# Kernel optimization log

Measured on AMD Instinct MI355X. Metric: run time of the kernel, lower is better.

Reference implementation:

```python
import jax, jax.numpy as jnp
import numpy as np

TEMPERATURE = 0.1
TIME_THRESHOLD = 365
NEG = -1e9  # stands in for -inf; exp(NEG - max) == 0 exactly in fp32
EPS = 1e-12  # F.normalize eps


def setup_inputs() -> dict:
    key = jax.random.key(0)
    k1, k2, k3 = jax.random.split(key, 3)
    B, D = 8192, 128
    embeddings = jax.random.normal(k1, (B, D), dtype=jnp.float32)
    survival_times = jax.random.randint(k2, (B,), 0, 3650, dtype=jnp.int32)
    censor = jax.random.randint(k3, (B,), 0, 2, dtype=jnp.int32)
    return {"embeddings": embeddings, "survival_times": survival_times, "censor": censor}


def reference(embeddings, survival_times, censor):
    B = embeddings.shape[0]
    # L2 normalize rows (torch F.normalize semantics)
    norm = jnp.maximum(jnp.linalg.norm(embeddings, axis=1, keepdims=True), EPS)
    z = embeddings / norm
    # pairwise cosine similarity / temperature: [B, B]
    sim = jnp.einsum('ik,jk->ij', z, z) / TEMPERATURE
    diag = jnp.eye(B, dtype=bool)
    sim = jnp.where(diag, NEG, sim)  # mask self-similarity
    # positive mask: |t_i - t_j| < threshold, i != j, row i uncensored
    tdiff = jnp.abs(survival_times[:, None] - survival_times[None, :])
    pos = (tdiff < TIME_THRESHOLD) & (~diag) & (censor[:, None] == 1)
    # per-row masked logsumexp reductions
    denominator = jax.nn.logsumexp(sim, axis=1)                      # [B]
    numerator = jax.nn.logsumexp(jnp.where(pos, sim, NEG), axis=1)   # [B]
    has_pos = jnp.any(pos, axis=1)
    per_row = jnp.where(has_pos, denominator - numerator, 0.0)
    cnt = jnp.sum(has_pos.astype(jnp.float32))
    return jnp.where(cnt > 0, jnp.sum(per_row) / jnp.maximum(cnt, 1.0), 0.0)
```

## Files before the change

kernel.cpp:

```cpp
#include <hip/hip_runtime.h>
#include <cstdint>

#define BDIM 8192
#define DDIM 128
#define JS 32

#define ZH_OFF 0
#define ZL_OFF (2 * 1024 * 1024)
#define RL_OFF (4 * 1024 * 1024)
#define CNT_OFF (RL_OFF + BDIM * 4)
#define FC_OFF (CNT_OFF + 64)
#define P_OFF (RL_OFF + 65536)
#define PART_OFF (P_OFF + BDIM * JS * 8)

typedef __attribute__((ext_vector_type(8))) short bf16x8;
typedef __attribute__((ext_vector_type(4))) float f32x4;

__device__ __forceinline__ short f2bf(float f) {
  unsigned u = __float_as_uint(f);
  unsigned r = (u + 0x7fffu + ((u >> 16) & 1u)) >> 16;
  return (short)r;
}
__device__ __forceinline__ float bf2f(short h) {
  return __uint_as_float(((unsigned)(unsigned short)h) << 16);
}
__device__ __forceinline__ void gload_lds16(const void* g, void* l) {
  __builtin_amdgcn_global_load_lds(
      (const __attribute__((address_space(1))) unsigned int*)g,
      (__attribute__((address_space(3))) unsigned int*)l, 16, 0, 0);
}


__global__ __launch_bounds__(256) void ck_prep(
    const float* __restrict__ emb, const int* __restrict__ censor,
    short* __restrict__ ZhT, short* __restrict__ ZlT,
    int* __restrict__ rowlist, int* __restrict__ cnt, int* __restrict__ fc)
{
  __shared__ float zl[16][132];
  __shared__ float pr[16][16];
  __shared__ float inv[16];
  __shared__ int wtot[4], woff[4];

  const int t = threadIdx.x;
  if (blockIdx.x == 512) {
    const int lane = t & 63, wv = t >> 6;
    const int4* c4 = (const int4*)(censor + t * 32);
    unsigned fm = 0;
#pragma unroll
    for (int q = 0; q < 8; ++q) {
      const int4 v = c4[q];
      fm |= (unsigned)(v.x == 1) << (q * 4 + 0);
      fm |= (unsigned)(v.y == 1) << (q * 4 + 1);
      fm |= (unsigned)(v.z == 1) << (q * 4 + 2);
      fm |= (unsigned)(v.w == 1) << (q * 4 + 3);
    }
    const int loc = __popc(fm);
    int sc = loc;
#pragma unroll
    for (int m = 1; m < 64; m <<= 1) {
      const int u = __shfl_up(sc, m, 64);
      if (lane >= m) sc += u;
    }
    if (lane == 63) wtot[wv] = sc;
    __syncthreads();
    if (t == 0) {
      int run = 0;
#pragma unroll
      for (int i = 0; i < 4; ++i) { woff[i] = run; run += wtot[i]; }
      fc[0] = 0;
    }
    __syncthreads();
    int off = woff[wv] + sc - loc;
    for (int u = 0; u < 32; ++u)
      if ((fm >> u) & 1) rowlist[off++] = t * 32 + u;
    if (t == 255) cnt[0] = off;
    return;
  }

  const int R = blockIdx.x;
  const int r16 = t >> 4, seg = t & 15;
  const float4* src = (const float4*)(emb + (size_t)(R * 16 + r16) * DDIM + seg * 8);
  const float4 v0 = src[0], v1 = src[1];
  float* zr = &zl[r16][seg * 8];
  zr[0] = v0.x; zr[1] = v0.y; zr[2] = v0.z; zr[3] = v0.w;
  zr[4] = v1.x; zr[5] = v1.y; zr[6] = v1.z; zr[7] = v1.w;
  pr[r16][seg] = v0.x * v0.x + v0.y * v0.y + v0.z * v0.z + v0.w * v0.w +
                 v1.x * v1.x + v1.y * v1.y + v1.z * v1.z + v1.w * v1.w;
  __syncthreads();
  if (t < 16) {
    float ss = 0.f;
#pragma unroll
    for (int s = 0; s < 16; ++s) ss += pr[t][s];
    inv[t] = 1.0f / fmaxf(sqrtf(ss), 1e-12f);
  }
  __syncthreads();
  const int kc = t >> 6, hf = (t >> 4) & 3, rw = t & 15;
  const float iv = inv[rw];
  const float* zs = &zl[rw][(kc * 4 + hf) * 8];
  short hs[8], ls[8];
#pragma unroll
  for (int j = 0; j < 8; ++j) {
    const float z = zs[j] * iv;
    const short h = f2bf(z);
    hs[j] = h;
    ls[j] = f2bf(z - bf2f(h));
  }
  const int dst = R * 2048 + t * 8;
  *(bf16x8*)(ZhT + dst) = *(const bf16x8*)hs;
  *(bf16x8*)(ZlT + dst) = *(const bf16x8*)ls;
}

__global__ __launch_bounds__(256, 2) void ck_main(
    const short* __restrict__ ZhT, const short* __restrict__ ZlT,
    const int* __restrict__ rowlist, const int* __restrict__ cntp,
    const int* __restrict__ times, float2* __restrict__ P2)
{
  __shared__ __align__(16) char lds[65536];
  const int cnt = *cntp;
  const int t = threadIdx.x;
  const int b = blockIdx.x;
  const int it = b >> 5;
  const int js = b & 31;
  if (it * 128 >= cnt) return;
  const int lane = t & 63;
  const int w = t >> 6;
  const int half = lane >> 4;
  const int ll = lane & 15;
  const int jR0 = js * 16;

  int rbase[2];
#pragma unroll
  for (int a = 0; a < 2; ++a) {
    int c = it * 128 + w * 32 + a * 16 + ll;
    if (c >= cnt) c = cnt - 1;
    const int r = rowlist[c];
    rbase[a] = (r >> 4) * 2048 + (r & 15) * 8;
  }
  bf16x8 ah[2][4];
#pragma unroll
  for (int a = 0; a < 2; ++a)
#pragma unroll
    for (int kc = 0; kc < 4; ++kc)
      ah[a][kc] = *(const bf16x8*)(ZhT + rbase[a] + kc * 512 + half * 128);

  int meta[2][4];
#pragma unroll
  for (int a = 0; a < 2; ++a)
#pragma unroll
    for (int r = 0; r < 4; ++r) {
      const int idx = it * 128 + w * 32 + a * 16 + half * 4 + r;
      const bool vi = idx < cnt;
      const int gi = rowlist[vi ? idx : 0];
      const int taP = vi ? (times[gi] + 364) : 50000;
      meta[a][r] = (taP << 16) | (vi ? gi : 0xFFFF);
    }

  float sd[2][4] = {{0.f}}, sn[2][4] = {{0.f}};

  {
    const int c0 = w * 8;
#pragma unroll
    for (int u = 0; u < 8; ++u) {
      const int c = c0 + u, cp = c & 15;
      const short* src = (c < 16) ? ZhT : ZlT;
      const short* gp = src + (size_t)(jR0 + (cp >> 2)) * 2048 + (cp & 3) * 512 + lane * 8;
      gload_lds16(gp, lds + ((c < 16) ? 0 : 16384) + cp * 1024);
    }
  }

  for (int st = 0; st < 4; ++st) {
    __syncthreads();
    if (st < 3) {
      const int pB = ((st + 1) & 1) * 32768;
      const int c0 = w * 8;
#pragma unroll
      for (int u = 0; u < 8; ++u) {
        const int c = c0 + u, cp = c & 15;
        const short* src = (c < 16) ? ZhT : ZlT;
        const short* gp = src + (size_t)(jR0 + (st + 1) * 4 + (cp >> 2)) * 2048 + (cp & 3) * 512 + lane * 8;
        gload_lds16(gp, lds + pB + ((c < 16) ? 0 : 16384) + cp * 1024);
      }
    }

    const char* L = lds + (st & 1) * 32768;
    f32x4 acc[2][4];
#pragma unroll
    for (int a = 0; a < 2; ++a)
#pragma unroll
      for (int bb = 0; bb < 4; ++bb) acc[a][bb] = (f32x4){0.f, 0.f, 0.f, 0.f};

#pragma unroll
    for (int kc = 0; kc < 4; ++kc) {
      bf16x8 alv[2];
#pragma unroll
      for (int a = 0; a < 2; ++a)
        alv[a] = *(const bf16x8*)(ZlT + rbase[a] + kc * 512 + half * 128);
#pragma unroll
      for (int bb = 0; bb < 4; ++bb) {
        const bf16x8 bhv = *(const bf16x8*)(L + bb * 4096 + kc * 1024 + lane * 16);
        const bf16x8 blv = *(const bf16x8*)(L + 16384 + bb * 4096 + kc * 1024 + lane * 16);
        acc[0][bb] = __builtin_amdgcn_mfma_f32_16x16x32_bf16(ah[0][kc], bhv, acc[0][bb], 0, 0, 0);
        acc[1][bb] = __builtin_amdgcn_mfma_f32_16x16x32_bf16(ah[1][kc], bhv, acc[1][bb], 0, 0, 0);
        acc[0][bb] = __builtin_amdgcn_mfma_f32_16x16x32_bf16(ah[0][kc], blv, acc[0][bb], 0, 0, 0);
        acc[1][bb] = __builtin_amdgcn_mfma_f32_16x16x32_bf16(ah[1][kc], blv, acc[1][bb], 0, 0, 0);
        acc[0][bb] = __builtin_amdgcn_mfma_f32_16x16x32_bf16(alv[0], bhv, acc[0][bb], 0, 0, 0);
        acc[1][bb] = __builtin_amdgcn_mfma_f32_16x16x32_bf16(alv[1], bhv, acc[1][bb], 0, 0, 0);
      }
    }

    const int jb = js * 256 + st * 64;
    int tJ[4];
#pragma unroll
    for (int bb = 0; bb < 4; ++bb) tJ[bb] = times[jb + bb * 16 + ll];
#pragma unroll
    for (int a = 0; a < 2; ++a)
#pragma unroll
      for (int r = 0; r < 4; ++r) {
        const int m_ = meta[a][r];
        const int gi = m_ & 0xFFFF;
        const unsigned taP = ((unsigned)m_) >> 16;
        float d = 0.f, n = 0.f;
#pragma unroll
        for (int bb = 0; bb < 4; ++bb) {
          const int jgb = jb + bb * 16 + ll;
          float pv = __expf(fmaf(acc[a][bb][r], 10.f, -10.f));
          pv = (gi == jgb) ? 0.f : pv;
          d += pv;
          n += ((unsigned)(taP - (unsigned)tJ[bb]) <= 728u) ? pv : 0.f;
        }
        sd[a][r] += d;
        sn[a][r] += n;
      }
  }

#pragma unroll
  for (int a = 0; a < 2; ++a)
#pragma unroll
    for (int r = 0; r < 4; ++r) {
      float d = sd[a][r], n = sn[a][r];
#pragma unroll
      for (int m = 1; m <= 8; m <<= 1) {
        d += __shfl_xor(d, m, 64);
        n += __shfl_xor(n, m, 64);
      }
      const int idx = it * 128 + w * 32 + a * 16 + half * 4 + r;
      if (ll == 0 && idx < cnt) P2[(size_t)idx * JS + js] = make_float2(d, n);
    }
}

__global__ __launch_bounds__(256) void ck_fin(
    const float2* __restrict__ P2, const int* __restrict__ cntp,
    float2* __restrict__ part, int* __restrict__ fc, float* __restrict__ out)
{
  const int cnt = *cntp;
  const int t = threadIdx.x;
  const int idx = blockIdx.x * 256 + t;
  float lsum = 0.f, lcnt = 0.f;
  if (idx < cnt) {
    const float4* p = (const float4*)(P2 + (size_t)idx * JS);
    float d = 0.f, n = 0.f;
#pragma unroll
    for (int u = 0; u < 16; ++u) {
      const float4 v = p[u];
      d += v.x + v.z;
      n += v.y + v.w;
    }
    if (n > 0.f) { lsum = logf(d) - logf(n); lcnt = 1.f; }
  }
  __shared__ float s1[256], s2[256];
  __shared__ int amLast;
  s1[t] = lsum; s2[t] = lcnt;
  __syncthreads();
  for (int s = 128; s > 0; s >>= 1) {
    if (t < s) { s1[t] += s1[t + s]; s2[t] += s2[t + s]; }
    __syncthreads();
  }
  if (t == 0) {
    part[blockIdx.x] = make_float2(s1[0], s2[0]);
    __threadfence();
    amLast = (atomicAdd(fc, 1) == gridDim.x - 1);
  }
  __syncthreads();
  if (amLast) {
    __threadfence();
    float s = 0.f, c = 0.f;
    if (t < 32) { const float2 v = part[t]; s = v.x; c = v.y; }
    if (t < 64) {
#pragma unroll
      for (int m = 1; m < 64; m <<= 1) {
        s += __shfl_xor(s, m, 64);
        c += __shfl_xor(c, m, 64);
      }
      if (t == 0) out[0] = (c > 0.f) ? s / fmaxf(c, 1.f) : 0.f;
    }
  }
}

extern "C" void kernel_launch(void* const* d_in, const int* in_sizes, int n_in,
                              void* d_out, int out_size, void* d_ws, size_t ws_size,
                              hipStream_t stream) {
  const float* emb  = (const float*)d_in[0];
  const int* times  = (const int*)d_in[1];
  const int* censor = (const int*)d_in[2];
  float* out = (float*)d_out;

  char* ws = (char*)d_ws;
  short* ZhT    = (short*)(ws + ZH_OFF);
  short* ZlT    = (short*)(ws + ZL_OFF);
  int* rowlist  = (int*)(ws + RL_OFF);
  int* cntp     = (int*)(ws + CNT_OFF);
  int* fc       = (int*)(ws + FC_OFF);
  float2* P2    = (float2*)(ws + P_OFF);
  float2* part  = (float2*)(ws + PART_OFF);

  ck_prep<<<513, 256, 0, stream>>>(emb, censor, ZhT, ZlT, rowlist, cntp, fc);
  ck_main<<<64 * 32, 256, 0, stream>>>(ZhT, ZlT, rowlist, cntp, times, P2);
  ck_fin<<<32, 256, 0, stream>>>(P2, cntp, part, fc, out);
}
```

Before: 111.6 us.

## Fuse final reduction into main kernel and halve column splits per row block

The finalize kernel is removed. Its work now runs in the last-arriving block of each row tile, found through per-tile atomic counters, and partial sums are combined with global float atomics plus a done counter. The column split drops from 32 to 16, so each block processes 512 columns over 8 pipeline stages, halving the grid and the partial-sum traffic. The patch also raises wave priority around the MFMA loop and uses exp2 with a prescaled constant instead of __expf. This saves a kernel launch and a pass over P2, but gives fewer blocks for the GPU's CUs and makes the result depend on the order of float atomics.

```diff
diff --git a/kernel.cpp b/kernel.cpp
--- a/kernel.cpp
+++ b/kernel.cpp
@@ -3,15 +3,16 @@
 
 #define BDIM 8192
 #define DDIM 128
-#define JS 32
+#define JS 16
 
 #define ZH_OFF 0
 #define ZL_OFF (2 * 1024 * 1024)
 #define RL_OFF (4 * 1024 * 1024)
 #define CNT_OFF (RL_OFF + BDIM * 4)
-#define FC_OFF (CNT_OFF + 64)
+#define IC_OFF (CNT_OFF + 64)
+#define DC_OFF (IC_OFF + 256)
+#define GS_OFF (DC_OFF + 64)
 #define P_OFF (RL_OFF + 65536)
-#define PART_OFF (P_OFF + BDIM * JS * 8)
 
 typedef __attribute__((ext_vector_type(8))) short bf16x8;
 typedef __attribute__((ext_vector_type(4))) float f32x4;
@@ -34,7 +35,9 @@
 __global__ __launch_bounds__(256) void ck_prep(
     const float* __restrict__ emb, const int* __restrict__ censor,
     short* __restrict__ ZhT, short* __restrict__ ZlT,
-    int* __restrict__ rowlist, int* __restrict__ cnt, int* __restrict__ fc)
+    int* __restrict__ rowlist, int* __restrict__ cnt,
+    int* __restrict__ ic, int* __restrict__ dc, float* __restrict__ gsc,
+    float* __restrict__ out)
 {
   __shared__ float zl[16][132];
   __shared__ float pr[16][16];
@@ -43,6 +46,9 @@
 
   const int t = threadIdx.x;
   if (blockIdx.x == 512) {
+    if (t < 64) ic[t] = 0;
+    if (t == 64) dc[0] = 0;
+    if (t == 65) { gsc[0] = 0.f; gsc[1] = 0.f; }
     const int lane = t & 63, wv = t >> 6;
     const int4* c4 = (const int4*)(censor + t * 32);
     unsigned fm = 0;
@@ -67,13 +73,15 @@
       int run = 0;
 #pragma unroll
       for (int i = 0; i < 4; ++i) { woff[i] = run; run += wtot[i]; }
-      fc[0] = 0;
     }
     __syncthreads();
     int off = woff[wv] + sc - loc;
     for (int u = 0; u < 32; ++u)
       if ((fm >> u) & 1) rowlist[off++] = t * 32 + u;
-    if (t == 255) cnt[0] = off;
+    if (t == 255) {
+      cnt[0] = off;
+      if (off == 0) out[0] = 0.f;
+    }
     return;
   }
 
@@ -113,20 +121,23 @@
 __global__ __launch_bounds__(256, 2) void ck_main(
     const short* __restrict__ ZhT, const short* __restrict__ ZlT,
     const int* __restrict__ rowlist, const int* __restrict__ cntp,
-    const int* __restrict__ times, float2* __restrict__ P2)
+    const int* __restrict__ times, float2* __restrict__ P2,
+    int* __restrict__ ic, int* __restrict__ dc, float* __restrict__ gsc,
+    float* __restrict__ out)
 {
   __shared__ __align__(16) char lds[65536];
+  __shared__ int lastFlag;
   const int cnt = *cntp;
   const int t = threadIdx.x;
   const int b = blockIdx.x;
-  const int it = b >> 5;
-  const int js = b & 31;
+  const int it = b >> 4;
+  const int js = b & 15;
   if (it * 128 >= cnt) return;
   const int lane = t & 63;
   const int w = t >> 6;
   const int half = lane >> 4;
   const int ll = lane & 15;
-  const int jR0 = js * 16;
+  const int jU0 = js * 32;
 
   int rbase[2];
 #pragma unroll
@@ -163,21 +174,21 @@
     for (int u = 0; u < 8; ++u) {
       const int c = c0 + u, cp = c & 15;
       const short* src = (c < 16) ? ZhT : ZlT;
-      const short* gp = src + (size_t)(jR0 + (cp >> 2)) * 2048 + (cp & 3) * 512 + lane * 8;
+      const short* gp = src + (size_t)(jU0 + (cp >> 2)) * 2048 + (cp & 3) * 512 + lane * 8;
       gload_lds16(gp, lds + ((c < 16) ? 0 : 16384) + cp * 1024);
     }
   }
 
-  for (int st = 0; st < 4; ++st) {
+  for (int st = 0; st < 8; ++st) {
     __syncthreads();
-    if (st < 3) {
+    if (st < 7) {
       const int pB = ((st + 1) & 1) * 32768;
       const int c0 = w * 8;
 #pragma unroll
       for (int u = 0; u < 8; ++u) {
         const int c = c0 + u, cp = c & 15;
         const short* src = (c < 16) ? ZhT : ZlT;
-        const short* gp = src + (size_t)(jR0 + (st + 1) * 4 + (cp >> 2)) * 2048 + (cp & 3) * 512 + lane * 8;
+        const short* gp = src + (size_t)(jU0 + (st + 1) * 4 + (cp >> 2)) * 2048 + (cp & 3) * 512 + lane * 8;
         gload_lds16(gp, lds + pB + ((c < 16) ? 0 : 16384) + cp * 1024);
       }
     }
@@ -189,6 +200,7 @@
 #pragma unroll
       for (int bb = 0; bb < 4; ++bb) acc[a][bb] = (f32x4){0.f, 0.f, 0.f, 0.f};
 
+    __builtin_amdgcn_s_setprio(1);
 #pragma unroll
     for (int kc = 0; kc < 4; ++kc) {
       bf16x8 alv[2];
@@ -207,8 +219,10 @@
         acc[1][bb] = __builtin_amdgcn_mfma_f32_16x16x32_bf16(alv[1], bhv, acc[1][bb], 0, 0, 0);
       }
     }
-
-    const int jb = js * 256 + st * 64;
+    __builtin_amdgcn_s_setprio(0);
+
+    const float K2 = 14.426950408889634f;
+    const int jb = js * 512 + st * 64;
     int tJ[4];
 #pragma unroll
     for (int bb = 0; bb < 4; ++bb) tJ[bb] = times[jb + bb * 16 + ll];
@@ -223,7 +237,7 @@
 #pragma unroll
         for (int bb = 0; bb < 4; ++bb) {
           const int jgb = jb + bb * 16 + ll;
-          float pv = __expf(fmaf(acc[a][bb][r], 10.f, -10.f));
+          float pv = __builtin_amdgcn_exp2f(fmaf(acc[a][bb][r], K2, -K2));
           pv = (gi == jgb) ? 0.f : pv;
           d += pv;
           n += ((unsigned)(taP - (unsigned)tJ[bb]) <= 728u) ? pv : 0.f;
@@ -246,52 +260,45 @@
       const int idx = it * 128 + w * 32 + a * 16 + half * 4 + r;
       if (ll == 0 && idx < cnt) P2[(size_t)idx * JS + js] = make_float2(d, n);
     }
-}
-
-__global__ __launch_bounds__(256) void ck_fin(
-    const float2* __restrict__ P2, const int* __restrict__ cntp,
-    float2* __restrict__ part, int* __restrict__ fc, float* __restrict__ out)
-{
-  const int cnt = *cntp;
-  const int t = threadIdx.x;
-  const int idx = blockIdx.x * 256 + t;
-  float lsum = 0.f, lcnt = 0.f;
-  if (idx < cnt) {
-    const float4* p = (const float4*)(P2 + (size_t)idx * JS);
+
+  __threadfence();
+  __syncthreads();
+  if (t == 0) lastFlag = (atomicAdd(&ic[it], 1) == JS - 1);
+  __syncthreads();
+  if (!lastFlag) return;
+  __threadfence();
+
+  const int r0 = it * 128;
+  const int rows = min(128, cnt - r0);
+  float ls = 0.f, lc = 0.f;
+  if (t < rows) {
+    const float4* p = (const float4*)(P2 + (size_t)(r0 + t) * JS);
     float d = 0.f, n = 0.f;
 #pragma unroll
-    for (int u = 0; u < 16; ++u) {
+    for (int u = 0; u < 8; ++u) {
       const float4 v = p[u];
       d += v.x + v.z;
       n += v.y + v.w;
     }
-    if (n > 0.f) { lsum = logf(d) - logf(n); lcnt = 1.f; }
-  }
-  __shared__ float s1[256], s2[256];
-  __shared__ int amLast;
-  s1[t] = lsum; s2[t] = lcnt;
+    if (n > 0.f) { ls = logf(d) - logf(n); lc = 1.f; }
+  }
+  float* s1 = (float*)lds;
+  float* s2 = s1 + 256;
+  s1[t] = ls; s2[t] = lc;
   __syncthreads();
   for (int s = 128; s > 0; s >>= 1) {
     if (t < s) { s1[t] += s1[t + s]; s2[t] += s2[t + s]; }
     __syncthreads();
   }
   if (t == 0) {
-    part[blockIdx.x] = make_float2(s1[0], s2[0]);
+    atomicAdd(&gsc[0], s1[0]);
+    atomicAdd(&gsc[1], s2[0]);
     __threadfence();
-    amLast = (atomicAdd(fc, 1) == gridDim.x - 1);
-  }
-  __syncthreads();
-  if (amLast) {
-    __threadfence();
-    float s = 0.f, c = 0.f;
-    if (t < 32) { const float2 v = part[t]; s = v.x; c = v.y; }
-    if (t < 64) {
-#pragma unroll
-      for (int m = 1; m < 64; m <<= 1) {
-        s += __shfl_xor(s, m, 64);
-        c += __shfl_xor(c, m, 64);
-      }
-      if (t == 0) out[0] = (c > 0.f) ? s / fmaxf(c, 1.f) : 0.f;
+    const int nAct = (cnt + 127) >> 7;
+    if (atomicAdd(dc, 1) == nAct - 1) {
+      const float s = atomicAdd(&gsc[0], 0.f);
+      const float c = atomicAdd(&gsc[1], 0.f);
+      out[0] = (c > 0.f) ? s / fmaxf(c, 1.f) : 0.f;
     }
   }
 }
@@ -309,11 +316,11 @@
   short* ZlT    = (short*)(ws + ZL_OFF);
   int* rowlist  = (int*)(ws + RL_OFF);
   int* cntp     = (int*)(ws + CNT_OFF);
-  int* fc       = (int*)(ws + FC_OFF);
+  int* ic       = (int*)(ws + IC_OFF);
+  int* dc       = (int*)(ws + DC_OFF);
+  float* gsc    = (float*)(ws + GS_OFF);
   float2* P2    = (float2*)(ws + P_OFF);
-  float2* part  = (float2*)(ws + PART_OFF);
-
-  ck_prep<<<513, 256, 0, stream>>>(emb, censor, ZhT, ZlT, rowlist, cntp, fc);
-  ck_main<<<64 * 32, 256, 0, stream>>>(ZhT, ZlT, rowlist, cntp, times, P2);
-  ck_fin<<<32, 256, 0, stream>>>(P2, cntp, part, fc, out);
-}
+
+  ck_prep<<<513, 256, 0, stream>>>(emb, censor, ZhT, ZlT, rowlist, cntp, ic, dc, gsc, out);
+  ck_main<<<64 * JS, 256, 0, stream>>>(ZhT, ZlT, rowlist, cntp, times, P2, ic, dc, gsc, out);
+}
```

New measurement: 152.9 us. 37.1% more time.
